# Performance work log

Measured on AMD Instinct MI355X. Metric: run time of the kernel, lower is better.

Reference implementation:

```python
import jax, jax.numpy as jnp
import numpy as np

NUM_TAGS = 3


def setup_inputs() -> dict:
    key = jax.random.key(0)
    k1, k2, k3 = jax.random.split(key, 3)
    B, T, K = 2048, 4096, NUM_TAGS
    logits = jax.random.normal(k1, (B, T, K), dtype=jnp.float32)
    transitions = jax.random.normal(k2, (K, K), dtype=jnp.float32)
    tags = jax.random.randint(k3, (B, T), 0, K, dtype=jnp.int64)
    return {"logits": logits, "transitions": transitions, "tags": tags}


def reference(logits, transitions, tags):
    """Negative CRF log-likelihood (AllenNLP CRF, include_start_end_transitions=False,
    full mask), i.e. -(sum_b [joint_score(b) - log_partition(b)])."""
    # --- log partition via forward algorithm (lax.scan over time) ---
    # alpha: [B, K]; emissions scanned over time: [T-1, B, K]
    def step(alpha, emit_t):
        # broadcast: alpha[b, i] + transitions[i, j] -> logsumexp over i
        new_alpha = jax.nn.logsumexp(alpha[:, :, None] + transitions[None, :, :], axis=1) + emit_t
        return new_alpha, None

    alpha0 = logits[:, 0, :]                              # [B, K]
    emits_rest = jnp.swapaxes(logits[:, 1:, :], 0, 1)     # [T-1, B, K]
    alpha_T, _ = jax.lax.scan(step, alpha0, emits_rest)
    log_z = jax.nn.logsumexp(alpha_T, axis=1)             # [B]

    # --- joint (numerator) score of the gold tag sequence ---
    emit_score = jnp.take_along_axis(logits, tags[:, :, None], axis=2)[..., 0].sum(axis=1)  # [B]
    trans_score = transitions[tags[:, :-1], tags[:, 1:]].sum(axis=1)                         # [B]

    loglik = emit_score + trans_score - log_z
    return -jnp.sum(loglik)
```

## Files before the change

kernel.cpp:

```cpp
#include <hip/hip_runtime.h>

#define BB 2048
#define TT 4096
#define LN2 0.69314718055994530942f

__global__ __launch_bounds__(512) void crf_pass1(
    const float* __restrict__ logits, const float* __restrict__ trans,
    const int* __restrict__ tags, float* __restrict__ ws)
{
    __shared__ float sTrans[9];
    __shared__ float sTrExp[9];
    __shared__ float sRec[7][12];
    const int tid = threadIdx.x;
    if (tid < 9) {
        float tv = trans[tid];
        sTrans[tid] = tv;
        sTrExp[tid] = __expf(tv);
    }
    __syncthreads();

    const int b = blockIdx.x;
    const int c = tid;

    const int4*   tp = (const int4*)(tags + (size_t)b * TT + (size_t)c * 8);
    const float4* lp = (const float4*)(logits + ((size_t)b * TT + (size_t)c * 8) * 3);

    int4 Tq0 = tp[0], Tq1 = tp[1];
    float Lf[24];
#pragma unroll
    for (int i = 0; i < 6; ++i) {
        float4 t = lp[i];
        Lf[4*i+0] = t.x; Lf[4*i+1] = t.y; Lf[4*i+2] = t.z; Lf[4*i+3] = t.w;
    }
    __builtin_amdgcn_sched_barrier(0);

    unsigned pk =  (unsigned)Tq0.x        | ((unsigned)Tq0.y << 2)
                | ((unsigned)Tq0.z << 4)  | ((unsigned)Tq0.w << 6)
                | ((unsigned)Tq1.x << 8)  | ((unsigned)Tq1.y << 10)
                | ((unsigned)Tq1.z << 12) | ((unsigned)Tq1.w << 14);

    const float t00 = sTrExp[0], t01 = sTrExp[1], t02 = sTrExp[2];
    const float t10 = sTrExp[3], t11 = sTrExp[4], t12 = sTrExp[5];
    const float t20 = sTrExp[6], t21 = sTrExp[7], t22 = sTrExp[8];

    float a00 = 1.f, a01 = 0.f, a02 = 0.f;
    float a10 = 0.f, a11 = 1.f, a12 = 0.f;
    float a20 = 0.f, a21 = 0.f, a22 = 1.f;
    int   se = 0;
    float score = 0.f;
    unsigned acc = 0u;
    int prev = 0;
    float v0 = 0.f, v1 = 0.f, v2 = 0.f;

#define MATSTEP(e0_, e1_, e2_) do {                                     \
    float x0 = __expf(e0_), x1 = __expf(e1_), x2 = __expf(e2_);         \
    float b0_ = (a00*t00 + a01*t10 + a02*t20) * x0;                     \
    float b1_ = (a00*t01 + a01*t11 + a02*t21) * x1;                     \
    float b2_ = (a00*t02 + a01*t12 + a02*t22) * x2;                     \
    float b3_ = (a10*t00 + a11*t10 + a12*t20) * x0;                     \
    float b4_ = (a10*t01 + a11*t11 + a12*t21) * x1;                     \
    float b5_ = (a10*t02 + a11*t12 + a12*t22) * x2;                     \
    float b6_ = (a20*t00 + a21*t10 + a22*t20) * x0;                     \
    float b7_ = (a20*t01 + a21*t11 + a22*t21) * x1;                     \
    float b8_ = (a20*t02 + a21*t12 + a22*t22) * x2;                     \
    a00=b0_; a01=b1_; a02=b2_; a10=b3_; a11=b4_; a12=b5_; a20=b6_; a21=b7_; a22=b8_; \
} while (0)

#define RENORM do {                                                     \
    float m_ = fmaxf(fmaxf(fmaxf(a00, a01), fmaxf(a02, a10)),           \
                     fmaxf(fmaxf(a11, a12), fmaxf(fmaxf(a20, a21), a22))); \
    int ef_ = (int)(__float_as_uint(m_) >> 23);                         \
    float scf_ = __uint_as_float((unsigned)(254 - ef_) << 23);          \
    se += ef_ - 127;                                                    \
    a00 *= scf_; a01 *= scf_; a02 *= scf_;                              \
    a10 *= scf_; a11 *= scf_; a12 *= scf_;                              \
    a20 *= scf_; a21 *= scf_; a22 *= scf_;                              \
} while (0)

#pragma unroll
    for (int s = 0; s < 8; ++s) {
        float e0 = Lf[3*s+0], e1 = Lf[3*s+1], e2 = Lf[3*s+2];
        int tg = (int)((pk >> (2*s)) & 3u);
        if (s == 0) {
            if (c == 0) {
                v0 = __expf(e0); v1 = __expf(e1); v2 = __expf(e2);
            } else {
                MATSTEP(e0, e1, e2);
            }
        } else {
            MATSTEP(e0, e1, e2);
            acc += 1u << (3 * (prev * 3 + tg));
        }
        score += (tg == 0) ? e0 : ((tg == 1) ? e1 : e2);
        prev = tg;
    }
    RENORM;

#pragma unroll
    for (int p = 0; p < 9; ++p)
        score += (float)((int)((acc >> (3 * p)) & 7u)) * sTrans[p];

    int fp = (int)(pk & 3u) | (prev << 8);
#pragma unroll
    for (int m = 1; m < 64; m <<= 1) {
        float o00 = __shfl_down(a00, m, 64), o01 = __shfl_down(a01, m, 64), o02 = __shfl_down(a02, m, 64);
        float o10 = __shfl_down(a10, m, 64), o11 = __shfl_down(a11, m, 64), o12 = __shfl_down(a12, m, 64);
        float o20 = __shfl_down(a20, m, 64), o21 = __shfl_down(a21, m, 64), o22 = __shfl_down(a22, m, 64);
        int   ose = __shfl_down(se, m, 64);
        float osc = __shfl_down(score, m, 64);
        int   ofp = __shfl_down(fp, m, 64);

        float c00 = a00*o00 + a01*o10 + a02*o20;
        float c01 = a00*o01 + a01*o11 + a02*o21;
        float c02 = a00*o02 + a01*o12 + a02*o22;
        float c10 = a10*o00 + a11*o10 + a12*o20;
        float c11 = a10*o01 + a11*o11 + a12*o21;
        float c12 = a10*o02 + a11*o12 + a12*o22;
        float c20 = a20*o00 + a21*o10 + a22*o20;
        float c21 = a20*o01 + a21*o11 + a22*o21;
        float c22 = a20*o02 + a21*o12 + a22*o22;

        score = score + osc + sTrans[(fp >> 8) * 3 + (ofp & 255)];
        fp = (fp & 255) | (ofp & ~255);
        se += ose;

        a00=c00; a01=c01; a02=c02; a10=c10; a11=c11; a12=c12; a20=c20; a21=c21; a22=c22;
        RENORM;
    }
    prev = fp >> 8;

    const int lane = tid & 63;
    const int wid  = tid >> 6;
    if (lane == 0 && wid > 0) {
        sRec[wid-1][0] = a00; sRec[wid-1][1] = a01; sRec[wid-1][2] = a02;
        sRec[wid-1][3] = a10; sRec[wid-1][4] = a11; sRec[wid-1][5] = a12;
        sRec[wid-1][6] = a20; sRec[wid-1][7] = a21; sRec[wid-1][8] = a22;
        sRec[wid-1][9]  = __int_as_float(se);
        sRec[wid-1][10] = score;
        sRec[wid-1][11] = __int_as_float(fp);
    }
    __syncthreads();
    if (tid == 0) {
#pragma unroll
        for (int k = 0; k < 7; ++k) {
            float m00 = sRec[k][0], m01 = sRec[k][1], m02 = sRec[k][2];
            float m10 = sRec[k][3], m11 = sRec[k][4], m12 = sRec[k][5];
            float m20 = sRec[k][6], m21 = sRec[k][7], m22 = sRec[k][8];
            int   shm = __float_as_int(sRec[k][9]);
            float scm = sRec[k][10];
            int   pkm = __float_as_int(sRec[k][11]);

            float c00 = a00*m00 + a01*m10 + a02*m20;
            float c01 = a00*m01 + a01*m11 + a02*m21;
            float c02 = a00*m02 + a01*m12 + a02*m22;
            float c10 = a10*m00 + a11*m10 + a12*m20;
            float c11 = a10*m01 + a11*m11 + a12*m21;
            float c12 = a10*m02 + a11*m12 + a12*m22;
            float c20 = a20*m00 + a21*m10 + a22*m20;
            float c21 = a20*m01 + a21*m11 + a22*m21;
            float c22 = a20*m02 + a21*m12 + a22*m22;

            score += scm + sTrans[prev * 3 + (pkm & 255)];
            prev = pkm >> 8;
            se += shm;
            a00=c00; a01=c01; a02=c02; a10=c10; a11=c11; a12=c12; a20=c20; a21=c21; a22=c22;
            RENORM;
        }
        float n0 = v0*a00 + v1*a10 + v2*a20;
        float n1 = v0*a01 + v1*a11 + v2*a21;
        float n2 = v0*a02 + v1*a12 + v2*a22;
        float logz = logf(n0 + n1 + n2) + (float)se * LN2;
        ws[b] = logz - score;
    }

#undef MATSTEP
#undef RENORM
}

__global__ __launch_bounds__(256) void crf_reduce(
    const float* __restrict__ ws, float* __restrict__ out)
{
    int tid = threadIdx.x;
    float s = 0.f;
#pragma unroll
    for (int k = 0; k < BB / 256; ++k) s += ws[k * 256 + tid];
    for (int off = 32; off > 0; off >>= 1) s += __shfl_down(s, off, 64);
    __shared__ float sP[4];
    if ((tid & 63) == 0) sP[tid >> 6] = s;
    __syncthreads();
    if (tid == 0) out[0] = sP[0] + sP[1] + sP[2] + sP[3];
}

extern "C" void kernel_launch(void* const* d_in, const int* in_sizes, int n_in,
                              void* d_out, int out_size, void* d_ws, size_t ws_size,
                              hipStream_t stream) {
    const float* logits = (const float*)d_in[0];
    const float* trans  = (const float*)d_in[1];
    const int*   tags   = (const int*)d_in[2];
    float* out = (float*)d_out;
    float* ws  = (float*)d_ws;

    crf_pass1<<<dim3(BB), dim3(512), 0, stream>>>(logits, trans, tags, ws);
    crf_reduce<<<dim3(1), dim3(256), 0, stream>>>(ws, out);
}
```

Measured before the change: 36.16 us.

## Replace wavefront shuffle reduction with DPP row-shift scan and precomputed boundary transitions

Replaces the ds_bpermute-based __shfl_down tree reduction of 3x3 transfer matrices with DPP row_shr/row_bcast inclusive-scan steps that reduce toward lane 63. Boundary transition scores between adjacent lanes are added once up front via a single shuffle, so each fold round no longer needs an LDS lookup. The cross-wave combine then runs on thread 511. The aim is to cut cross-lane latency and LDS traffic in the reduction. The scan-style DPP pattern and its data-dependent bound_ctrl semantics are subtle, which makes correctness a risk.

```diff
diff --git a/kernel.cpp b/kernel.cpp
--- a/kernel.cpp
+++ b/kernel.cpp
@@ -3,6 +3,16 @@
 #define BB 2048
 #define TT 4096
 #define LN2 0.69314718055994530942f
+
+template<int CTRL>
+__device__ __forceinline__ float dppf(float x) {
+    return __int_as_float(__builtin_amdgcn_update_dpp(
+        0, __float_as_int(x), CTRL, 0xF, 0xF, true));
+}
+template<int CTRL>
+__device__ __forceinline__ int dppi(int x) {
+    return __builtin_amdgcn_update_dpp(0, x, CTRL, 0xF, 0xF, true);
+}
 
 __global__ __launch_bounds__(512) void crf_pass1(
     const float* __restrict__ logits, const float* __restrict__ trans,
@@ -11,6 +21,7 @@
     __shared__ float sTrans[9];
     __shared__ float sTrExp[9];
     __shared__ float sRec[7][12];
+    __shared__ float sV[3];
     const int tid = threadIdx.x;
     if (tid < 9) {
         float tv = trans[tid];
@@ -100,49 +111,78 @@
     for (int p = 0; p < 9; ++p)
         score += (float)((int)((acc >> (3 * p)) & 7u)) * sTrans[p];
 
-    int fp = (int)(pk & 3u) | (prev << 8);
-#pragma unroll
-    for (int m = 1; m < 64; m <<= 1) {
-        float o00 = __shfl_down(a00, m, 64), o01 = __shfl_down(a01, m, 64), o02 = __shfl_down(a02, m, 64);
-        float o10 = __shfl_down(a10, m, 64), o11 = __shfl_down(a11, m, 64), o12 = __shfl_down(a12, m, 64);
-        float o20 = __shfl_down(a20, m, 64), o21 = __shfl_down(a21, m, 64), o22 = __shfl_down(a22, m, 64);
-        int   ose = __shfl_down(se, m, 64);
-        float osc = __shfl_down(score, m, 64);
-        int   ofp = __shfl_down(fp, m, 64);
-
-        float c00 = a00*o00 + a01*o10 + a02*o20;
-        float c01 = a00*o01 + a01*o11 + a02*o21;
-        float c02 = a00*o02 + a01*o12 + a02*o22;
-        float c10 = a10*o00 + a11*o10 + a12*o20;
-        float c11 = a10*o01 + a11*o11 + a12*o21;
-        float c12 = a10*o02 + a11*o12 + a12*o22;
-        float c20 = a20*o00 + a21*o10 + a22*o20;
-        float c21 = a20*o01 + a21*o11 + a22*o21;
-        float c22 = a20*o02 + a21*o12 + a22*o22;
-
-        score = score + osc + sTrans[(fp >> 8) * 3 + (ofp & 255)];
-        fp = (fp & 255) | (ofp & ~255);
-        se += ose;
-
-        a00=c00; a01=c01; a02=c02; a10=c10; a11=c11; a12=c12; a20=c20; a21=c21; a22=c22;
-        RENORM;
-    }
-    prev = fp >> 8;
-
     const int lane = tid & 63;
     const int wid  = tid >> 6;
-    if (lane == 0 && wid > 0) {
-        sRec[wid-1][0] = a00; sRec[wid-1][1] = a01; sRec[wid-1][2] = a02;
-        sRec[wid-1][3] = a10; sRec[wid-1][4] = a11; sRec[wid-1][5] = a12;
-        sRec[wid-1][6] = a20; sRec[wid-1][7] = a21; sRec[wid-1][8] = a22;
-        sRec[wid-1][9]  = __int_as_float(se);
-        sRec[wid-1][10] = score;
-        sRec[wid-1][11] = __int_as_float(fp);
-    }
+
+    {
+        int opv = __shfl_up(prev, 1, 64);
+        if (lane != 0) score += sTrans[opv * 3 + (int)(pk & 3u)];
+    }
+
+    int fp = (int)(pk & 3u) | (prev << 8);
+
+#define FOLD_ROUND(CTRL) do {                                           \
+    float o00=dppf<CTRL>(a00), o01=dppf<CTRL>(a01), o02=dppf<CTRL>(a02);\
+    float o10=dppf<CTRL>(a10), o11=dppf<CTRL>(a11), o12=dppf<CTRL>(a12);\
+    float o20=dppf<CTRL>(a20), o21=dppf<CTRL>(a21), o22=dppf<CTRL>(a22);\
+    int   ose=dppi<CTRL>(se);                                           \
+    float osc=dppf<CTRL>(score);                                        \
+    int   ofp=dppi<CTRL>(fp);                                           \
+    float c00=o00*a00+o01*a10+o02*a20;                                  \
+    float c01=o00*a01+o01*a11+o02*a21;                                  \
+    float c02=o00*a02+o01*a12+o02*a22;                                  \
+    float c10=o10*a00+o11*a10+o12*a20;                                  \
+    float c11=o10*a01+o11*a11+o12*a21;                                  \
+    float c12=o10*a02+o11*a12+o12*a22;                                  \
+    float c20=o20*a00+o21*a10+o22*a20;                                  \
+    float c21=o20*a01+o21*a11+o22*a21;                                  \
+    float c22=o20*a02+o21*a12+o22*a22;                                  \
+    score += osc; se += ose;                                            \
+    fp = (ofp & 255) | (fp & 0xFF00);                                   \
+    a00=c00; a01=c01; a02=c02; a10=c10; a11=c11; a12=c12;               \
+    a20=c20; a21=c21; a22=c22;                                          \
+    RENORM;                                                             \
+} while (0)
+
+    FOLD_ROUND(0x111);
+    FOLD_ROUND(0x112);
+    FOLD_ROUND(0x114);
+    FOLD_ROUND(0x118);
+    FOLD_ROUND(0x142);
+    FOLD_ROUND(0x143);
+
+    if (lane == 63 && wid < 7) {
+        sRec[wid][0] = a00; sRec[wid][1] = a01; sRec[wid][2] = a02;
+        sRec[wid][3] = a10; sRec[wid][4] = a11; sRec[wid][5] = a12;
+        sRec[wid][6] = a20; sRec[wid][7] = a21; sRec[wid][8] = a22;
+        sRec[wid][9]  = __int_as_float(se);
+        sRec[wid][10] = score;
+        sRec[wid][11] = __int_as_float(fp);
+    }
+    if (tid == 0) { sV[0] = v0; sV[1] = v1; sV[2] = v2; }
     __syncthreads();
-    if (tid == 0) {
-#pragma unroll
-        for (int k = 0; k < 7; ++k) {
+
+    if (tid == 511) {
+        float p00 = sRec[0][0], p01 = sRec[0][1], p02 = sRec[0][2];
+        float p10 = sRec[0][3], p11 = sRec[0][4], p12 = sRec[0][5];
+        float p20 = sRec[0][6], p21 = sRec[0][7], p22 = sRec[0][8];
+        int   seT   = __float_as_int(sRec[0][9]);
+        float scT   = sRec[0][10];
+        int   lastT = __float_as_int(sRec[0][11]) >> 8;
+
+#define RENORMP do {                                                    \
+    float m_ = fmaxf(fmaxf(fmaxf(p00, p01), fmaxf(p02, p10)),           \
+                     fmaxf(fmaxf(p11, p12), fmaxf(fmaxf(p20, p21), p22))); \
+    int ef_ = (int)(__float_as_uint(m_) >> 23);                         \
+    float scf_ = __uint_as_float((unsigned)(254 - ef_) << 23);          \
+    seT += ef_ - 127;                                                   \
+    p00 *= scf_; p01 *= scf_; p02 *= scf_;                              \
+    p10 *= scf_; p11 *= scf_; p12 *= scf_;                              \
+    p20 *= scf_; p21 *= scf_; p22 *= scf_;                              \
+} while (0)
+
+#pragma unroll
+        for (int k = 1; k < 7; ++k) {
             float m00 = sRec[k][0], m01 = sRec[k][1], m02 = sRec[k][2];
             float m10 = sRec[k][3], m11 = sRec[k][4], m12 = sRec[k][5];
             float m20 = sRec[k][6], m21 = sRec[k][7], m22 = sRec[k][8];
@@ -150,31 +190,51 @@
             float scm = sRec[k][10];
             int   pkm = __float_as_int(sRec[k][11]);
 
-            float c00 = a00*m00 + a01*m10 + a02*m20;
-            float c01 = a00*m01 + a01*m11 + a02*m21;
-            float c02 = a00*m02 + a01*m12 + a02*m22;
-            float c10 = a10*m00 + a11*m10 + a12*m20;
-            float c11 = a10*m01 + a11*m11 + a12*m21;
-            float c12 = a10*m02 + a11*m12 + a12*m22;
-            float c20 = a20*m00 + a21*m10 + a22*m20;
-            float c21 = a20*m01 + a21*m11 + a22*m21;
-            float c22 = a20*m02 + a21*m12 + a22*m22;
-
-            score += scm + sTrans[prev * 3 + (pkm & 255)];
-            prev = pkm >> 8;
-            se += shm;
-            a00=c00; a01=c01; a02=c02; a10=c10; a11=c11; a12=c12; a20=c20; a21=c21; a22=c22;
-            RENORM;
+            float c00 = p00*m00 + p01*m10 + p02*m20;
+            float c01 = p00*m01 + p01*m11 + p02*m21;
+            float c02 = p00*m02 + p01*m12 + p02*m22;
+            float c10 = p10*m00 + p11*m10 + p12*m20;
+            float c11 = p10*m01 + p11*m11 + p12*m21;
+            float c12 = p10*m02 + p11*m12 + p12*m22;
+            float c20 = p20*m00 + p21*m10 + p22*m20;
+            float c21 = p20*m01 + p21*m11 + p22*m21;
+            float c22 = p20*m02 + p21*m12 + p22*m22;
+
+            scT += scm + sTrans[lastT * 3 + (pkm & 255)];
+            lastT = pkm >> 8;
+            seT  += shm;
+            p00=c00; p01=c01; p02=c02; p10=c10; p11=c11; p12=c12;
+            p20=c20; p21=c21; p22=c22;
+            RENORMP;
         }
-        float n0 = v0*a00 + v1*a10 + v2*a20;
-        float n1 = v0*a01 + v1*a11 + v2*a21;
-        float n2 = v0*a02 + v1*a12 + v2*a22;
-        float logz = logf(n0 + n1 + n2) + (float)se * LN2;
-        ws[b] = logz - score;
+        {
+            float c00 = p00*a00 + p01*a10 + p02*a20;
+            float c01 = p00*a01 + p01*a11 + p02*a21;
+            float c02 = p00*a02 + p01*a12 + p02*a22;
+            float c10 = p10*a00 + p11*a10 + p12*a20;
+            float c11 = p10*a01 + p11*a11 + p12*a21;
+            float c12 = p10*a02 + p11*a12 + p12*a22;
+            float c20 = p20*a00 + p21*a10 + p22*a20;
+            float c21 = p20*a01 + p21*a11 + p22*a21;
+            float c22 = p20*a02 + p21*a12 + p22*a22;
+
+            scT += score + sTrans[lastT * 3 + (fp & 255)];
+            seT += se;
+            p00=c00; p01=c01; p02=c02; p10=c10; p11=c11; p12=c12;
+            p20=c20; p21=c21; p22=c22;
+        }
+        float w0 = sV[0], w1 = sV[1], w2 = sV[2];
+        float n0 = w0*p00 + w1*p10 + w2*p20;
+        float n1 = w0*p01 + w1*p11 + w2*p21;
+        float n2 = w0*p02 + w1*p12 + w2*p22;
+        float logz = logf(n0 + n1 + n2) + (float)seT * LN2;
+        ws[b] = logz - scT;
+#undef RENORMP
     }
 
 #undef MATSTEP
 #undef RENORM
+#undef FOLD_ROUND
 }
 
 __global__ __launch_bounds__(256) void crf_reduce(
```

Result: faster. 32.59 us (-9.9%).
